# Performance work log

Measured on AMD Instinct MI355X. Metric: run time of the kernel, lower is better.

## Reference

```python
import jax, jax.numpy as jnp
import numpy as np

B, C, H, W = 8, 256, 64, 64
HEADS, R, TOPK_FRAC = 8, 4, 0.25
DIM = C // HEADS
SCALE = DIM ** -0.5


def setup_inputs() -> dict:
    key = jax.random.key(0)
    ks = jax.random.split(key, 8)
    s = 0.05
    return {
        "x": jax.random.normal(ks[0], (B, C, H, W), jnp.float32),
        "w_q": jax.random.normal(ks[1], (C, C), jnp.float32) * s,
        "w_k": jax.random.normal(ks[2], (C, C), jnp.float32) * s,
        "w_v": jax.random.normal(ks[3], (C, C), jnp.float32) * s,
        "w_ck": jax.random.normal(ks[4], (C, R, R), jnp.float32) * s,  # depthwise kxk
        "w_cv": jax.random.normal(ks[5], (C, R, R), jnp.float32) * s,
        "w_out": jax.random.normal(ks[6], (C, C), jnp.float32) * s,
        "b_out": jax.random.normal(ks[7], (C,), jnp.float32) * s,
    }


def _conv1x1(x, w):
    # x: [B,C,H,W], w: [O,C]
    return jnp.einsum('bchw,oc->bohw', x, w)


def _depthwise_pool(x, w):
    # depthwise conv, kernel=stride=R -> non-overlapping blocks
    b, c, h, wd = x.shape
    blocks = x.reshape(b, c, h // R, R, wd // R, R)
    return jnp.einsum('bcirjs,crs->bcij', blocks, w)


def reference(x, w_q, w_k, w_v, w_ck, w_cv, w_out, b_out):
    N = H * W
    q = _conv1x1(x, w_q)
    k = _conv1x1(x, w_k)
    v = _conv1x1(x, w_v)
    k_s = _depthwise_pool(k, w_ck)   # [B,C,H/R,W/R]
    v_s = _depthwise_pool(v, w_cv)
    n = k_s.shape[2] * k_s.shape[3]

    BH = B * HEADS
    q = q.reshape(B, HEADS, DIM, N).reshape(BH, DIM, N)
    k = k_s.reshape(B, HEADS, DIM, n).reshape(BH, DIM, n)
    v = v_s.reshape(B, HEADS, DIM, n).reshape(BH, DIM, n)

    # stage 1: full queries vs compressed keys
    attn = jax.nn.softmax(jnp.einsum('bdi,bdj->bij', q, k) * SCALE, axis=-1)
    token_score = attn.sum(axis=1)                     # [BH, n]
    top_k = max(1, int(n * TOPK_FRAC))
    _, idx = jax.lax.top_k(token_score, top_k)         # [BH, top_k]

    idx_exp = jnp.broadcast_to(idx[:, None, :], (BH, DIM, top_k))
    k_top = jnp.take_along_axis(k, idx_exp, axis=2)    # [BH, DIM, top_k]
    v_top = jnp.take_along_axis(v, idx_exp, axis=2)

    # stage 2: attend only to selected compressed tokens
    attn_full = jax.nn.softmax(jnp.einsum('bdi,bdj->bij', q, k_top) * SCALE, axis=-1)
    out = jnp.einsum('bij,bdj->bdi', attn_full, v_top)  # [BH, DIM, N]
    out = out.reshape(B, HEADS, DIM, N).reshape(B, C, H, W)
    return _conv1x1(out, w_out) + b_out[None, :, None, None]
```

## Files before the change

kernel.cpp:

```cpp
#include <hip/hip_runtime.h>

#define Bq 8
#define Cq 256
#define Hq 64
#define Wq 64
#define Nq 4096
#define HEADSq 8
#define DIMq 32
#define NCq 256
#define TOPKq 64
#define BHq 64
#define SCALEq 0.17677669529663687f

typedef short bf16x8 __attribute__((ext_vector_type(8)));
typedef float f32x4  __attribute__((ext_vector_type(4)));
typedef float f32x16 __attribute__((ext_vector_type(16)));

__device__ __forceinline__ uint32_t f2bf_hi(float f) {
  uint32_t u = __float_as_uint(f);
  return (u + 0x7FFFu + ((u >> 16) & 1u)) >> 16;
}

__device__ __forceinline__ void split8(const float* v, uint4& hv, uint4& lv) {
  uint32_t h[8], l[8];
#pragma unroll
  for (int j = 0; j < 8; ++j) {
    uint32_t hb = f2bf_hi(v[j]);
    float rest = v[j] - __uint_as_float(hb << 16);
    h[j] = hb;
    l[j] = __float_as_uint(rest) >> 16;
  }
  hv = make_uint4(h[0] | (h[1] << 16), h[2] | (h[3] << 16),
                  h[4] | (h[5] << 16), h[6] | (h[7] << 16));
  lv = make_uint4(l[0] | (l[1] << 16), l[2] | (l[3] << 16),
                  l[4] | (l[5] << 16), l[6] | (l[7] << 16));
}


__global__ __launch_bounds__(256) void prep_w(
    const float* __restrict__ wq, const float* __restrict__ wk,
    const float* __restrict__ wv, const float* __restrict__ wo,
    char* __restrict__ wt) {
  const int oblk = blockIdx.x, s = blockIdx.y, mat = blockIdx.z;
  const float* w = mat == 0 ? wq : mat == 1 ? wk : mat == 2 ? wv : wo;
  const int t = threadIdx.x;
  const int o = t & 63, g = t >> 6;
  float v[8];
  const float* src = w + (size_t)(oblk * 64 + o) * Cq + s * 32 + g * 8;
#pragma unroll
  for (int j = 0; j < 8; ++j) v[j] = src[j];
  uint4 hv, lv;
  split8(v, hv, lv);
  size_t base = ((size_t)((mat * 4 + oblk) * 8 + s)) * 8192;
  int off = ((o >> 5) * 2 + (g >> 1)) * 1024 + ((o & 31) + 32 * (g & 1)) * 16;
  *(uint4*)(wt + base + off) = hv;
  *(uint4*)(wt + base + 4096 + off) = lv;
}

__global__ __launch_bounds__(128) void prep_w32(
    const float* __restrict__ wq, const float* __restrict__ wk,
    const float* __restrict__ wv, char* __restrict__ wt32) {
  const int oblk = blockIdx.x, s = blockIdx.y, mat = blockIdx.z;
  const float* w = mat == 0 ? wq : mat == 1 ? wk : wv;
  const int t = threadIdx.x;
  const int o = t & 31, g = t >> 5;
  float v[8];
  const float* src = w + (size_t)(oblk * 32 + o) * Cq + s * 32 + g * 8;
#pragma unroll
  for (int j = 0; j < 8; ++j) v[j] = src[j];
  uint4 hv, lv;
  split8(v, hv, lv);
  size_t base = ((size_t)((mat * 8 + oblk) * 8 + s)) * 4096;
  int off = (g >> 1) * 1024 + (o + 32 * (g & 1)) * 16;
  *(uint4*)(wt32 + base + off) = hv;
  *(uint4*)(wt32 + base + 2048 + off) = lv;
}

__global__ __launch_bounds__(256) void prep_x(
    const float* __restrict__ x, char* __restrict__ xt) {
  const int n64 = blockIdx.x, s = blockIdx.y, b = blockIdx.z;
  const int t = threadIdx.x;
  __shared__ float xf[32][64];
  const float* xb = x + ((size_t)(b * Cq + s * 32)) * Nq + n64 * 64;
#pragma unroll
  for (int ii = 0; ii < 2; ++ii) {
    int e = t + ii * 256;
    int cl = e >> 4, n4 = (e & 15) * 4;
    *(float4*)&xf[cl][n4] = *(const float4*)&xb[(size_t)cl * Nq + n4];
  }
  __syncthreads();
  int n = t & 63, g = t >> 6;
  float v[8];
#pragma unroll
  for (int j = 0; j < 8; ++j) v[j] = xf[g * 8 + j][n];
  uint4 hv, lv;
  split8(v, hv, lv);
  char* dst = xt + ((size_t)((b * 8 + s) * 128 + n64 * 2 + (n >> 5))) * 4096;
  int off = (g >> 1) * 1024 + ((n & 31) + 32 * (g & 1)) * 16;
  *(uint4*)(dst + off) = hv;
  *(uint4*)(dst + 2048 + off) = lv;
}

__global__ __launch_bounds__(256) void qkv_fused(
    const char* __restrict__ wt32, const char* __restrict__ xt,
    const float* __restrict__ wck, const float* __restrict__ wcv,
    char* __restrict__ qimg, float* __restrict__ ksc, float* __restrict__ vsc,
    char* __restrict__ kim) {
  const int i = blockIdx.x, oblk = blockIdx.y, b = blockIdx.z;
  const int t = threadIdx.x, l = t & 63, wid = t >> 6;
  __shared__ __align__(16) short wimg[3][2][1024];
  __shared__ float pp[4][2][32][16];
  __shared__ float wpool[2][32][16];

  for (int u = t; u < 1024; u += 256) {
    int m = u >> 9, c = (u >> 4) & 31, e = u & 15;
    wpool[m][c][e] = (m ? wcv : wck)[(oblk * 32 + c) * 16 + e];
  }

  f32x16 acc[3][2];
#pragma unroll
  for (int m = 0; m < 3; ++m)
#pragma unroll
    for (int nt = 0; nt < 2; ++nt)
#pragma unroll
      for (int r = 0; r < 16; ++r) acc[m][nt][r] = 0.f;

  for (int s = 0; s < 8; ++s) {
    __syncthreads();
#pragma unroll
    for (int u = 0; u < 3; ++u) {
      int e = t + u * 256;
      int m = e >> 8, r = e & 255;
      ((uint4*)&wimg[m][0][0])[r] =
          ((const uint4*)(wt32 + ((size_t)((m * 8 + oblk) * 8 + s)) * 4096))[r];
    }
    __syncthreads();
    bf16x8 xh[2][2], xl[2][2];
#pragma unroll
    for (int nt = 0; nt < 2; ++nt) {
      const char* xb = xt + ((size_t)((b * 8 + s) * 128 + i * 8 + wid * 2 + nt)) * 4096;
#pragma unroll
      for (int kh = 0; kh < 2; ++kh) {
        int off = kh * 1024 + l * 16;
        xh[nt][kh] = *(const bf16x8*)(xb + off);
        xl[nt][kh] = *(const bf16x8*)(xb + 2048 + off);
      }
    }
#pragma unroll
    for (int m = 0; m < 3; ++m)
#pragma unroll
      for (int kh = 0; kh < 2; ++kh) {
        int off = kh * 1024 + l * 16;
        bf16x8 ah = *(const bf16x8*)((const char*)&wimg[m][0][0] + off);
        bf16x8 al = *(const bf16x8*)((const char*)&wimg[m][1][0] + off);
#pragma unroll
        for (int nt = 0; nt < 2; ++nt) {
          acc[m][nt] = __builtin_amdgcn_mfma_f32_32x32x16_bf16(ah, xh[nt][kh], acc[m][nt], 0, 0, 0);
          acc[m][nt] = __builtin_amdgcn_mfma_f32_32x32x16_bf16(ah, xl[nt][kh], acc[m][nt], 0, 0, 0);
          acc[m][nt] = __builtin_amdgcn_mfma_f32_32x32x16_bf16(al, xh[nt][kh], acc[m][nt], 0, 0, 0);
        }
      }
  }

#pragma unroll
  for (int m = 1; m <= 2; ++m)
#pragma unroll
    for (int nt = 0; nt < 2; ++nt)
#pragma unroll
      for (int r = 0; r < 16; ++r) {
        int c_l = (r & 3) + 8 * (r >> 2) + 4 * (l >> 5);
        float sv = acc[m][nt][r] * wpool[m - 1][c_l][wid * 4 + (l & 3)];
        float t0 = sv + __shfl_xor(sv, 1);
        float s4 = t0 + __shfl_xor(t0, 2);
        if ((l & 3) == 0)
          pp[wid][m - 1][c_l][nt * 8 + ((l & 31) >> 2)] = s4;
      }

  const int bh = b * 8 + oblk;
  {
    char* qb = qimg + ((size_t)(bh * 64 + i * 4 + wid)) * 8192;
    const int hi = l >> 5;
#pragma unroll
    for (int nt = 0; nt < 2; ++nt) {
      float sw[16];
#pragma unroll
      for (int r = 0; r < 16; ++r) sw[r] = __shfl_xor(acc[0][nt][r], 32);
      float e0[8], e1[8];
#pragma unroll
      for (int j = 0; j < 4; ++j) {
        e0[j]     = hi ? sw[4 + j]          : acc[0][nt][j];
        e0[4 + j] = hi ? acc[0][nt][4 + j]  : sw[j];
        e1[j]     = hi ? sw[12 + j]         : acc[0][nt][8 + j];
        e1[4 + j] = hi ? acc[0][nt][12 + j] : sw[8 + j];
      }
      uint4 h0, l0v, h1, l1v;
      split8(e0, h0, l0v);
      split8(e1, h1, l1v);
      *(uint4*)(qb + (nt * 2) * 1024 + l * 16) = h0;
      *(uint4*)(qb + 4096 + (nt * 2) * 1024 + l * 16) = l0v;
      *(uint4*)(qb + (nt * 2 + 1) * 1024 + l * 16) = h1;
      *(uint4*)(qb + 4096 + (nt * 2 + 1) * 1024 + l * 16) = l1v;
    }
  }
  __syncthreads();
  float* kpool = &wpool[0][0][0];
  float* vpool = &wpool[1][0][0];
  {
    int c = t >> 3, jj = t & 7;
#pragma unroll
    for (int m = 0; m < 2; ++m)
#pragma unroll
      for (int rep = 0; rep < 2; ++rep) {
        int j = jj + rep * 8;
        float v = pp[0][m][c][j] + pp[1][m][c][j] + pp[2][m][c][j] + pp[3][m][c][j];
        (m ? vpool : kpool)[c * 16 + j] = v;
        float* dst = m ? vsc : ksc;
        dst[((size_t)b * Cq + oblk * 32 + c) * NCq + i * 16 + j] = v;
      }
  }
  __syncthreads();
  if (t < 64) {
    int j = l & 15, g = l >> 4;
    float v[8];
#pragma unroll
    for (int jj = 0; jj < 8; ++jj) v[jj] = kpool[(g * 8 + jj) * 16 + j];
    uint4 hv, lv;
    split8(v, hv, lv);
    char* kb = kim + (size_t)bh * 32768 + i * 1024 + l * 16;
    *(uint4*)kb = hv;
    *(uint4*)(kb + 16384) = lv;
  }
}

__global__ __launch_bounds__(256) void stage1_mfma(
    const char* __restrict__ qim, const char* __restrict__ kim,
    float* __restrict__ part) {
  const int bh = blockIdx.y, chunk = blockIdx.x;
  const int t = threadIdx.x, l = t & 63, wid = t >> 6;
  __shared__ __align__(16) char kimgL[32768];
  __shared__ float sc[4][256];

  {
    const uint4* src = (const uint4*)(kim + (size_t)bh * 32768);
#pragma unroll
    for (int ii = 0; ii < 8; ++ii)
      ((uint4*)kimgL)[t + ii * 256] = src[t + ii * 256];
  }
  float scoreacc[16];
#pragma unroll
  for (int tt = 0; tt < 16; ++tt) scoreacc[tt] = 0.f;
  const int aoff = ((wid >> 1) * 2 + (l >> 5)) * 1024 +
                   ((wid & 1) * 16 + (l & 15) + 32 * ((l >> 4) & 1)) * 16;
  __syncthreads();

#pragma unroll 1
  for (int step = 0; step < 4; ++step) {
    const char* qb = qim + ((size_t)(bh * 64 + chunk * 4 + step)) * 8192;
    bf16x8 ah = *(const bf16x8*)(qb + aoff);
    bf16x8 al = *(const bf16x8*)(qb + 4096 + aoff);
    f32x4 acc[16];
#pragma unroll
    for (int tt = 0; tt < 16; ++tt)
#pragma unroll
      for (int r = 0; r < 4; ++r) acc[tt][r] = 0.f;
#pragma unroll
    for (int tt = 0; tt < 16; ++tt) {
      bf16x8 bhf = *(const bf16x8*)(kimgL + tt * 1024 + l * 16);
      bf16x8 blf = *(const bf16x8*)(kimgL + 16384 + tt * 1024 + l * 16);
      acc[tt] = __builtin_amdgcn_mfma_f32_16x16x32_bf16(ah, bhf, acc[tt], 0, 0, 0);
      acc[tt] = __builtin_amdgcn_mfma_f32_16x16x32_bf16(ah, blf, acc[tt], 0, 0, 0);
      acc[tt] = __builtin_amdgcn_mfma_f32_16x16x32_bf16(al, bhf, acc[tt], 0, 0, 0);
    }
    float mx[4], sm[4];
#pragma unroll
    for (int r = 0; r < 4; ++r) {
      float m = acc[0][r];
#pragma unroll
      for (int tt = 1; tt < 16; ++tt) m = fmaxf(m, acc[tt][r]);
      mx[r] = m;
    }
#pragma unroll
    for (int off = 1; off < 16; off <<= 1)
#pragma unroll
      for (int r = 0; r < 4; ++r) mx[r] = fmaxf(mx[r], __shfl_xor(mx[r], off));
#pragma unroll
    for (int r = 0; r < 4; ++r) sm[r] = 0.f;
#pragma unroll
    for (int tt = 0; tt < 16; ++tt)
#pragma unroll
      for (int r = 0; r < 4; ++r) {
        float e = __expf((acc[tt][r] - mx[r]) * SCALEq);
        acc[tt][r] = e;
        sm[r] += e;
      }
#pragma unroll
    for (int off = 1; off < 16; off <<= 1)
#pragma unroll
      for (int r = 0; r < 4; ++r) sm[r] += __shfl_xor(sm[r], off);
#pragma unroll
    for (int r = 0; r < 4; ++r) sm[r] = 1.0f / sm[r];
#pragma unroll
    for (int tt = 0; tt < 16; ++tt) {
      float tp = acc[tt][0] * sm[0] + acc[tt][1] * sm[1] +
                 acc[tt][2] * sm[2] + acc[tt][3] * sm[3];
      tp += __shfl_xor(tp, 16);
      tp += __shfl_xor(tp, 32);
      scoreacc[tt] += tp;
    }
  }
  if (l < 16) {
#pragma unroll
    for (int tt = 0; tt < 16; ++tt) sc[wid][tt * 16 + l] = scoreacc[tt];
  }
  __syncthreads();
  {
    float v = sc[0][t] + sc[1][t] + sc[2][t] + sc[3][t];
    part[((size_t)bh * 16 + chunk) * NCq + t] = v;
  }
}

__global__ __launch_bounds__(256) void reduce_scores(
    const float* __restrict__ part, float* __restrict__ score) {
  int bh = blockIdx.x, t = threadIdx.x;
  float s = 0.f;
#pragma unroll
  for (int c = 0; c < 16; ++c) s += part[((size_t)bh * 16 + c) * NCq + t];
  score[bh * NCq + t] = s;
}

__global__ __launch_bounds__(256) void topk_sel(
    const float* __restrict__ score, int* __restrict__ idx) {
  int bh = blockIdx.x, t = threadIdx.x;
  __shared__ float s[NCq];
  s[t] = score[bh * NCq + t];
  __syncthreads();
  float st = s[t];
  int rank = 0;
  for (int j = 0; j < NCq; ++j) {
    float sj = s[j];
    rank += (sj > st) || (sj == st && j < t);
  }
  if (rank < TOPKq) idx[bh * TOPKq + rank] = t;
}

__global__ __launch_bounds__(256, 2) void stage2_mfma(
    const char* __restrict__ qim, const float* __restrict__ ks,
    const float* __restrict__ vs, const int* __restrict__ idx,
    char* __restrict__ at) {
  const int bh = blockIdx.y, b = bh >> 3, h = bh & 7;
  const int t = threadIdx.x, l = t & 63, wid = t >> 6;
  __shared__ __align__(16) short kimg[2][2048];
  __shared__ __align__(16) short vimg[2][2][1024];
  __shared__ float pbuf[128][66];
  __shared__ int ibs[64];

  bf16x8 ah[2], al[2];
  {
    const char* qb = qim + ((size_t)(bh * 64 + blockIdx.x * 2 + (wid >> 1))) * 8192;
#pragma unroll
    for (int kd = 0; kd < 2; ++kd) {
      int off = ((wid & 1) * 2 + kd) * 1024 + l * 16;
      ah[kd] = *(const bf16x8*)(qb + off);
      al[kd] = *(const bf16x8*)(qb + 4096 + off);
    }
  }
  const float* ksb = ks + ((size_t)b * Cq + h * DIMq) * NCq;
  const float* vsb = vs + ((size_t)b * Cq + h * DIMq) * NCq;
  if (t < 64) ibs[t] = idx[bh * TOPKq + t];
  __syncthreads();

  {
    int tok = t & 63, dg = t >> 6;
    int ti = ibs[tok];
    float v[8];
#pragma unroll
    for (int j = 0; j < 8; ++j) v[j] = ksb[(size_t)(dg * 8 + j) * NCq + ti];
    uint4 hv, lv;
    split8(v, hv, lv);
    int off = ((tok >> 5) * 2 + (dg >> 1)) * 1024 + ((tok & 31) + 32 * (dg & 1)) * 16;
    *(uint4*)((char*)&kimg[0][0] + off) = hv;
    *(uint4*)((char*)&kimg[1][0] + off) = lv;
  }
  {
    int d = l & 31, tko = l >> 5, img = (t >> 6) >> 1, kreg = (t >> 6) & 1;
    float v[8];
#pragma unroll
    for (int j = 0; j < 8; ++j) {
      int tok = img * 32 + kreg * 16 + tko * 8 + j;
      v[j] = vsb[(size_t)d * NCq + ibs[tok]];
    }
    uint4 hv, lv;
    split8(v, hv, lv);
    int off = kreg * 1024 + (d + 32 * tko) * 16;
    *(uint4*)((char*)&vimg[0][img][0] + off) = hv;
    *(uint4*)((char*)&vimg[1][img][0] + off) = lv;
  }
  __syncthreads();

  f32x16 pacc[2];
#pragma unroll
  for (int g = 0; g < 2; ++g)
#pragma unroll
    for (int r = 0; r < 16; ++r) pacc[g][r] = 0.f;
#pragma unroll
  for (int g = 0; g < 2; ++g)
#pragma unroll
    for (int kd = 0; kd < 2; ++kd) {
      int off = (g * 2 + kd) * 1024 + l * 16;
      bf16x8 bhf = *(const bf16x8*)((const char*)&kimg[0][0] + off);
      bf16x8 blf = *(const bf16x8*)((const char*)&kimg[1][0] + off);
      pacc[g] = __builtin_amdgcn_mfma_f32_32x32x16_bf16(ah[kd], bhf, pacc[g], 0, 0, 0);
      pacc[g] = __builtin_amdgcn_mfma_f32_32x32x16_bf16(ah[kd], blf, pacc[g], 0, 0, 0);
      pacc[g] = __builtin_amdgcn_mfma_f32_32x32x16_bf16(al[kd], bhf, pacc[g], 0, 0, 0);
    }
  {
    float mx[16], sm[16];
#pragma unroll
    for (int r = 0; r < 16; ++r) mx[r] = fmaxf(pacc[0][r], pacc[1][r]);
#pragma unroll
    for (int off = 1; off < 32; off <<= 1)
#pragma unroll
      for (int r = 0; r < 16; ++r) mx[r] = fmaxf(mx[r], __shfl_xor(mx[r], off));
#pragma unroll
    for (int r = 0; r < 16; ++r) {
      float e0 = __expf((pacc[0][r] - mx[r]) * SCALEq);
      float e1 = __expf((pacc[1][r] - mx[r]) * SCALEq);
      pacc[0][r] = e0; pacc[1][r] = e1;
      sm[r] = e0 + e1;
    }
#pragma unroll
    for (int off = 1; off < 32; off <<= 1)
#pragma unroll
      for (int r = 0; r < 16; ++r) sm[r] += __shfl_xor(sm[r], off);
#pragma unroll
    for (int r = 0; r < 16; ++r) sm[r] = 1.0f / sm[r];
#pragma unroll
    for (int g = 0; g < 2; ++g)
#pragma unroll
      for (int r = 0; r < 16; ++r) {
        int qrow = wid * 32 + (r & 3) + 8 * (r >> 2) + 4 * (l >> 5);
        pbuf[qrow][g * 32 + (l & 31)] = pacc[g][r] * sm[r];
      }
  }
  __syncthreads();
  f32x16 oacc;
#pragma unroll
  for (int r = 0; r < 16; ++r) oacc[r] = 0.f;
#pragma unroll
  for (int ks4 = 0; ks4 < 4; ++ks4) {
    const float* pa = &pbuf[wid * 32 + (l & 31)][ks4 * 16 + (l >> 5) * 8];
    float v[8];
#pragma unroll
    for (int j = 0; j < 8; ++j) v[j] = pa[j];
    uint4 hv, lv;
    split8(v, hv, lv);
    bf16x8 pah = *(const bf16x8*)&hv, pal = *(const bf16x8*)&lv;
    int off = (ks4 & 1) * 1024 + l * 16;
    bf16x8 bhf = *(const bf16x8*)((const char*)&vimg[0][ks4 >> 1][0] + off);
    bf16x8 blf = *(const bf16x8*)((const char*)&vimg[1][ks4 >> 1][0] + off);
    oacc = __builtin_amdgcn_mfma_f32_32x32x16_bf16(pah, bhf, oacc, 0, 0, 0);
    oacc = __builtin_amdgcn_mfma_f32_32x32x16_bf16(pah, blf, oacc, 0, 0, 0);
    oacc = __builtin_amdgcn_mfma_f32_32x32x16_bf16(pal, bhf, oacc, 0, 0, 0);
  }
#pragma unroll
  for (int r = 0; r < 16; ++r) {
    int qrow = wid * 32 + (r & 3) + 8 * (r >> 2) + 4 * (l >> 5);
    pbuf[qrow][l & 31] = oacc[r];
  }
  __syncthreads();
#pragma unroll
  for (int ii = 0; ii < 2; ++ii) {
    int slot = t + ii * 256;
    int row = slot >> 2, dg = slot & 3;
    float v[8];
#pragma unroll
    for (int j = 0; j < 8; ++j) v[j] = pbuf[row][dg * 8 + j];
    uint4 hv, lv;
    split8(v, hv, lv);
    int nb = blockIdx.x * 2 + (row >> 6), nloc = row & 63;
    size_t base = ((size_t)((b * 64 + nb) * 8 + h)) * 8192;
    int off = ((nloc >> 5) * 2 + (dg >> 1)) * 1024 +
              ((nloc & 31) + 32 * (dg & 1)) * 16;
    *(uint4*)(at + base + off) = hv;
    *(uint4*)(at + base + 4096 + off) = lv;
  }
}

__global__ __launch_bounds__(256) void out_mfma(
    const char* __restrict__ at, const char* __restrict__ wt,
    const float* __restrict__ bo, float* __restrict__ y) {
  const int b = blockIdx.z, oblk = blockIdx.y, nblk = blockIdx.x;
  const int o0 = oblk * 64, n0 = nblk * 64;
  const int t = threadIdx.x, l = t & 63, wid = t >> 6;
  const int ob = wid >> 1, nbw = wid & 1;
  __shared__ __align__(16) short wimg[2][2048];
  __shared__ __align__(16) short ximg[2][2048];
  __shared__ float bs[64];
  if (t < 64) bs[t] = bo[o0 + t];
  f32x16 acc;
#pragma unroll
  for (int i = 0; i < 16; ++i) acc[i] = 0.f;

  for (int s = 0; s < 8; ++s) {
    __syncthreads();
    {
      const uint4* srcw = (const uint4*)(wt + ((size_t)((12 + oblk) * 8 + s)) * 8192);
      const uint4* srcx = (const uint4*)(at + ((size_t)((b * 64 + nblk) * 8 + s)) * 8192);
#pragma unroll
      for (int i = 0; i < 2; ++i) {
        ((uint4*)&wimg[0][0])[t + i * 256] = srcw[t + i * 256];
        ((uint4*)&ximg[0][0])[t + i * 256] = srcx[t + i * 256];
      }
    }
    __syncthreads();
#pragma unroll
    for (int kh = 0; kh < 2; ++kh) {
      int offa = (ob * 2 + kh) * 1024 + l * 16;
      int offb = (nbw * 2 + kh) * 1024 + l * 16;
      bf16x8 ah = *(const bf16x8*)((const char*)&wimg[0][0] + offa);
      bf16x8 al = *(const bf16x8*)((const char*)&wimg[1][0] + offa);
      bf16x8 bhf = *(const bf16x8*)((const char*)&ximg[0][0] + offb);
      bf16x8 blf = *(const bf16x8*)((const char*)&ximg[1][0] + offb);
      acc = __builtin_amdgcn_mfma_f32_32x32x16_bf16(ah, bhf, acc, 0, 0, 0);
      acc = __builtin_amdgcn_mfma_f32_32x32x16_bf16(ah, blf, acc, 0, 0, 0);
      acc = __builtin_amdgcn_mfma_f32_32x32x16_bf16(al, bhf, acc, 0, 0, 0);
    }
  }
#pragma unroll
  for (int r = 0; r < 16; ++r) {
    int ol = ob * 32 + (r & 3) + 8 * (r >> 2) + 4 * (l >> 5);
    y[((size_t)(b * Cq + o0 + ol)) * Nq + n0 + nbw * 32 + (l & 31)] = acc[r] + bs[ol];
  }
}

extern "C" void kernel_launch(void* const* d_in, const int* in_sizes, int n_in,
                              void* d_out, int out_size, void* d_ws, size_t ws_size,
                              hipStream_t stream) {
  const float* x   = (const float*)d_in[0];
  const float* wq  = (const float*)d_in[1];
  const float* wk  = (const float*)d_in[2];
  const float* wv  = (const float*)d_in[3];
  const float* wck = (const float*)d_in[4];
  const float* wcv = (const float*)d_in[5];
  const float* wo  = (const float*)d_in[6];
  const float* bo  = (const float*)d_in[7];
  float* out = (float*)d_out;

  char* wsb = (char*)d_ws;
  char*  qimg = wsb;
  char*  xt   = wsb + ((size_t)32 << 20);
  char*  at   = xt;
  char*  wt   = wsb + ((size_t)64 << 20);
  char*  wt32 = wsb + ((size_t)65 << 20);
  char*  kim  = wsb + ((size_t)66 << 20);
  float* ksc  = (float*)(wsb + ((size_t)68 << 20));
  float* vsc  = (float*)(wsb + ((size_t)70 << 20));
  float* part = (float*)(wsb + ((size_t)72 << 20));
  float* score= (float*)(wsb + ((size_t)73 << 20));
  int*   idx  = (int*)(wsb + ((size_t)73 << 20) + 65536);

  prep_w<<<dim3(4, 8, 4), 256, 0, stream>>>(wq, wk, wv, wo, wt);
  prep_w32<<<dim3(8, 8, 3), 128, 0, stream>>>(wq, wk, wv, wt32);
  prep_x<<<dim3(64, 8, 8), 256, 0, stream>>>(x, xt);
  qkv_fused<<<dim3(16, 8, 8), 256, 0, stream>>>(wt32, xt, wck, wcv, qimg, ksc, vsc, kim);
  stage1_mfma<<<dim3(16, BHq), 256, 0, stream>>>(qimg, kim, part);
  reduce_scores<<<dim3(BHq), 256, 0, stream>>>(part, score);
  topk_sel<<<dim3(BHq), 256, 0, stream>>>(score, idx);
  stage2_mfma<<<dim3(32, BHq), 256, 0, stream>>>(qimg, ksc, vsc, idx, at);
  out_mfma<<<dim3(64, 4, 8), 256, 0, stream>>>(at, wt, bo, out);
}
```

Measured before the change: 178.5 us.

## Double-buffer weight and activation tiles in QKV and output GEMM kernels

Turns the shared-memory weight tiles in qkv_fused and out_mfma into two-slot ping-pong buffers, and prefetches the next K-slice of weights and activations (into registers for qkv) while MFMAs run on the current slice. Each iteration now needs one barrier instead of two, and global load latency can overlap with matrix math. The cost is doubled LDS for those tiles and extra registers for the prefetched x fragments, which may reduce occupancy. The hi/lo split precision scheme is unchanged.

```diff
diff --git a/kernel.cpp b/kernel.cpp
--- a/kernel.cpp
+++ b/kernel.cpp
@@ -108,7 +108,7 @@
     char* __restrict__ kim) {
   const int i = blockIdx.x, oblk = blockIdx.y, b = blockIdx.z;
   const int t = threadIdx.x, l = t & 63, wid = t >> 6;
-  __shared__ __align__(16) short wimg[3][2][1024];
+  __shared__ __align__(16) short wimg[2][3][2][1024];
   __shared__ float pp[4][2][32][16];
   __shared__ float wpool[2][32][16];
 
@@ -125,40 +125,69 @@
 #pragma unroll
       for (int r = 0; r < 16; ++r) acc[m][nt][r] = 0.f;
 
+  bf16x8 xh[2][2], xl[2][2], nxh[2][2], nxl[2][2];
+#pragma unroll
+  for (int u = 0; u < 3; ++u) {
+    int e = t + u * 256;
+    int m = e >> 8, r = e & 255;
+    ((uint4*)&wimg[0][m][0][0])[r] =
+        ((const uint4*)(wt32 + ((size_t)((m * 8 + oblk) * 8 + 0)) * 4096))[r];
+  }
+#pragma unroll
+  for (int nt = 0; nt < 2; ++nt) {
+    const char* xb = xt + ((size_t)((b * 8 + 0) * 128 + i * 8 + wid * 2 + nt)) * 4096;
+#pragma unroll
+    for (int kh = 0; kh < 2; ++kh) {
+      int off = kh * 1024 + l * 16;
+      xh[nt][kh] = *(const bf16x8*)(xb + off);
+      xl[nt][kh] = *(const bf16x8*)(xb + 2048 + off);
+    }
+  }
+  __syncthreads();
+
+#pragma unroll 1
   for (int s = 0; s < 8; ++s) {
-    __syncthreads();
-#pragma unroll
-    for (int u = 0; u < 3; ++u) {
-      int e = t + u * 256;
-      int m = e >> 8, r = e & 255;
-      ((uint4*)&wimg[m][0][0])[r] =
-          ((const uint4*)(wt32 + ((size_t)((m * 8 + oblk) * 8 + s)) * 4096))[r];
-    }
-    __syncthreads();
-    bf16x8 xh[2][2], xl[2][2];
-#pragma unroll
-    for (int nt = 0; nt < 2; ++nt) {
-      const char* xb = xt + ((size_t)((b * 8 + s) * 128 + i * 8 + wid * 2 + nt)) * 4096;
+    const int cur = s & 1;
+    if (s < 7) {
+#pragma unroll
+      for (int u = 0; u < 3; ++u) {
+        int e = t + u * 256;
+        int m = e >> 8, r = e & 255;
+        ((uint4*)&wimg[cur ^ 1][m][0][0])[r] =
+            ((const uint4*)(wt32 + ((size_t)((m * 8 + oblk) * 8 + s + 1)) * 4096))[r];
+      }
+#pragma unroll
+      for (int nt = 0; nt < 2; ++nt) {
+        const char* xb = xt + ((size_t)((b * 8 + s + 1) * 128 + i * 8 + wid * 2 + nt)) * 4096;
+#pragma unroll
+        for (int kh = 0; kh < 2; ++kh) {
+          int off = kh * 1024 + l * 16;
+          nxh[nt][kh] = *(const bf16x8*)(xb + off);
+          nxl[nt][kh] = *(const bf16x8*)(xb + 2048 + off);
+        }
+      }
+    }
+#pragma unroll
+    for (int m = 0; m < 3; ++m)
 #pragma unroll
       for (int kh = 0; kh < 2; ++kh) {
         int off = kh * 1024 + l * 16;
-        xh[nt][kh] = *(const bf16x8*)(xb + off);
-        xl[nt][kh] = *(const bf16x8*)(xb + 2048 + off);
-      }
-    }
-#pragma unroll
-    for (int m = 0; m < 3; ++m)
-#pragma unroll
-      for (int kh = 0; kh < 2; ++kh) {
-        int off = kh * 1024 + l * 16;
-        bf16x8 ah = *(const bf16x8*)((const char*)&wimg[m][0][0] + off);
-        bf16x8 al = *(const bf16x8*)((const char*)&wimg[m][1][0] + off);
+        bf16x8 ah = *(const bf16x8*)((const char*)&wimg[cur][m][0][0] + off);
+        bf16x8 al = *(const bf16x8*)((const char*)&wimg[cur][m][1][0] + off);
 #pragma unroll
         for (int nt = 0; nt < 2; ++nt) {
           acc[m][nt] = __builtin_amdgcn_mfma_f32_32x32x16_bf16(ah, xh[nt][kh], acc[m][nt], 0, 0, 0);
           acc[m][nt] = __builtin_amdgcn_mfma_f32_32x32x16_bf16(ah, xl[nt][kh], acc[m][nt], 0, 0, 0);
           acc[m][nt] = __builtin_amdgcn_mfma_f32_32x32x16_bf16(al, xh[nt][kh], acc[m][nt], 0, 0, 0);
         }
+      }
+    __syncthreads();
+#pragma unroll
+    for (int nt = 0; nt < 2; ++nt)
+#pragma unroll
+      for (int kh = 0; kh < 2; ++kh) {
+        xh[nt][kh] = nxh[nt][kh];
+        xl[nt][kh] = nxl[nt][kh];
       }
   }
 
@@ -493,38 +522,50 @@
   const int o0 = oblk * 64, n0 = nblk * 64;
   const int t = threadIdx.x, l = t & 63, wid = t >> 6;
   const int ob = wid >> 1, nbw = wid & 1;
-  __shared__ __align__(16) short wimg[2][2048];
-  __shared__ __align__(16) short ximg[2][2048];
+  __shared__ __align__(16) short wimg[2][2][2048];
+  __shared__ __align__(16) short ximg[2][2][2048];
   __shared__ float bs[64];
   if (t < 64) bs[t] = bo[o0 + t];
   f32x16 acc;
 #pragma unroll
   for (int i = 0; i < 16; ++i) acc[i] = 0.f;
 
+  {
+    const uint4* srcw = (const uint4*)(wt + ((size_t)((12 + oblk) * 8 + 0)) * 8192);
+    const uint4* srcx = (const uint4*)(at + ((size_t)((b * 64 + nblk) * 8 + 0)) * 8192);
+#pragma unroll
+    for (int i = 0; i < 2; ++i) {
+      ((uint4*)&wimg[0][0][0])[t + i * 256] = srcw[t + i * 256];
+      ((uint4*)&ximg[0][0][0])[t + i * 256] = srcx[t + i * 256];
+    }
+  }
+  __syncthreads();
+
+#pragma unroll 1
   for (int s = 0; s < 8; ++s) {
-    __syncthreads();
-    {
-      const uint4* srcw = (const uint4*)(wt + ((size_t)((12 + oblk) * 8 + s)) * 8192);
-      const uint4* srcx = (const uint4*)(at + ((size_t)((b * 64 + nblk) * 8 + s)) * 8192);
+    const int cur = s & 1;
+    if (s < 7) {
+      const uint4* srcw = (const uint4*)(wt + ((size_t)((12 + oblk) * 8 + s + 1)) * 8192);
+      const uint4* srcx = (const uint4*)(at + ((size_t)((b * 64 + nblk) * 8 + s + 1)) * 8192);
 #pragma unroll
       for (int i = 0; i < 2; ++i) {
-        ((uint4*)&wimg[0][0])[t + i * 256] = srcw[t + i * 256];
-        ((uint4*)&ximg[0][0])[t + i * 256] = srcx[t + i * 256];
-      }
-    }
-    __syncthreads();
+        ((uint4*)&wimg[cur ^ 1][0][0])[t + i * 256] = srcw[t + i * 256];
+        ((uint4*)&ximg[cur ^ 1][0][0])[t + i * 256] = srcx[t + i * 256];
+      }
+    }
 #pragma unroll
     for (int kh = 0; kh < 2; ++kh) {
       int offa = (ob * 2 + kh) * 1024 + l * 16;
       int offb = (nbw * 2 + kh) * 1024 + l * 16;
-      bf16x8 ah = *(const bf16x8*)((const char*)&wimg[0][0] + offa);
-      bf16x8 al = *(const bf16x8*)((const char*)&wimg[1][0] + offa);
-      bf16x8 bhf = *(const bf16x8*)((const char*)&ximg[0][0] + offb);
-      bf16x8 blf = *(const bf16x8*)((const char*)&ximg[1][0] + offb);
+      bf16x8 ah = *(const bf16x8*)((const char*)&wimg[cur][0][0] + offa);
+      bf16x8 al = *(const bf16x8*)((const char*)&wimg[cur][1][0] + offa);
+      bf16x8 bhf = *(const bf16x8*)((const char*)&ximg[cur][0][0] + offb);
+      bf16x8 blf = *(const bf16x8*)((const char*)&ximg[cur][1][0] + offb);
       acc = __builtin_amdgcn_mfma_f32_32x32x16_bf16(ah, bhf, acc, 0, 0, 0);
       acc = __builtin_amdgcn_mfma_f32_32x32x16_bf16(ah, blf, acc, 0, 0, 0);
       acc = __builtin_amdgcn_mfma_f32_32x32x16_bf16(al, bhf, acc, 0, 0, 0);
     }
+    __syncthreads();
   }
 #pragma unroll
   for (int r = 0; r < 16; ++r) {
```

After: 182.1 us. +2.0%, slower.

## Fuse score reduction into top-k and restructure out projection loads

Applied to the files above, without the earlier changes.

Merges the reduce_scores and topk_sel kernels into a single reduce_topk kernel, which removes one launch and the global round trip of the score buffer. The out_mfma kernel now loads all activation fragments straight from global memory into registers up front. It stages the weight tile through shared memory in two halves instead of syncing twice on every k-step. This cuts synchronisation and LDS traffic but raises register pressure (128 bf16x8 values per thread), which may reduce occupancy.

```diff
diff --git a/kernel.cpp b/kernel.cpp
--- a/kernel.cpp
+++ b/kernel.cpp
@@ -319,20 +319,14 @@
   }
 }
 
-__global__ __launch_bounds__(256) void reduce_scores(
-    const float* __restrict__ part, float* __restrict__ score) {
-  int bh = blockIdx.x, t = threadIdx.x;
-  float s = 0.f;
-#pragma unroll
-  for (int c = 0; c < 16; ++c) s += part[((size_t)bh * 16 + c) * NCq + t];
-  score[bh * NCq + t] = s;
-}
-
-__global__ __launch_bounds__(256) void topk_sel(
-    const float* __restrict__ score, int* __restrict__ idx) {
+__global__ __launch_bounds__(256) void reduce_topk(
+    const float* __restrict__ part, int* __restrict__ idx) {
   int bh = blockIdx.x, t = threadIdx.x;
   __shared__ float s[NCq];
-  s[t] = score[bh * NCq + t];
+  float v = 0.f;
+#pragma unroll
+  for (int c = 0; c < 16; ++c) v += part[((size_t)bh * 16 + c) * NCq + t];
+  s[t] = v;
   __syncthreads();
   float st = s[t];
   int rank = 0;
@@ -493,38 +487,66 @@
   const int o0 = oblk * 64, n0 = nblk * 64;
   const int t = threadIdx.x, l = t & 63, wid = t >> 6;
   const int ob = wid >> 1, nbw = wid & 1;
-  __shared__ __align__(16) short wimg[2][2048];
-  __shared__ __align__(16) short ximg[2][2048];
+  __shared__ __align__(16) char wimg[4][8192];
   __shared__ float bs[64];
   if (t < 64) bs[t] = bo[o0 + t];
+
   f32x16 acc;
 #pragma unroll
   for (int i = 0; i < 16; ++i) acc[i] = 0.f;
 
+  bf16x8 xh[8][2], xl[8][2];
+  const size_t atbase = ((size_t)((b * 64 + nblk) * 8)) * 8192;
+  const int offb0 = (nbw * 2 + 0) * 1024 + l * 16;
+  const int offb1 = (nbw * 2 + 1) * 1024 + l * 16;
+#pragma unroll
   for (int s = 0; s < 8; ++s) {
-    __syncthreads();
-    {
-      const uint4* srcw = (const uint4*)(wt + ((size_t)((12 + oblk) * 8 + s)) * 8192);
-      const uint4* srcx = (const uint4*)(at + ((size_t)((b * 64 + nblk) * 8 + s)) * 8192);
-#pragma unroll
-      for (int i = 0; i < 2; ++i) {
-        ((uint4*)&wimg[0][0])[t + i * 256] = srcw[t + i * 256];
-        ((uint4*)&ximg[0][0])[t + i * 256] = srcx[t + i * 256];
-      }
-    }
-    __syncthreads();
-#pragma unroll
-    for (int kh = 0; kh < 2; ++kh) {
-      int offa = (ob * 2 + kh) * 1024 + l * 16;
-      int offb = (nbw * 2 + kh) * 1024 + l * 16;
-      bf16x8 ah = *(const bf16x8*)((const char*)&wimg[0][0] + offa);
-      bf16x8 al = *(const bf16x8*)((const char*)&wimg[1][0] + offa);
-      bf16x8 bhf = *(const bf16x8*)((const char*)&ximg[0][0] + offb);
-      bf16x8 blf = *(const bf16x8*)((const char*)&ximg[1][0] + offb);
-      acc = __builtin_amdgcn_mfma_f32_32x32x16_bf16(ah, bhf, acc, 0, 0, 0);
-      acc = __builtin_amdgcn_mfma_f32_32x32x16_bf16(ah, blf, acc, 0, 0, 0);
-      acc = __builtin_amdgcn_mfma_f32_32x32x16_bf16(al, bhf, acc, 0, 0, 0);
-    }
+    const char* xb = at + atbase + (size_t)s * 8192;
+    xh[s][0] = *(const bf16x8*)(xb + offb0);
+    xh[s][1] = *(const bf16x8*)(xb + offb1);
+    xl[s][0] = *(const bf16x8*)(xb + 4096 + offb0);
+    xl[s][1] = *(const bf16x8*)(xb + 4096 + offb1);
+  }
+  const uint4* wsrc = (const uint4*)(wt + ((size_t)((12 + oblk) * 8)) * 8192);
+#pragma unroll
+  for (int u = 0; u < 8; ++u)
+    ((uint4*)&wimg[0][0])[t + u * 256] = wsrc[t + u * 256];
+  __syncthreads();
+
+  const int offa0 = (ob * 2 + 0) * 1024 + l * 16;
+  const int offa1 = (ob * 2 + 1) * 1024 + l * 16;
+#pragma unroll
+  for (int s = 0; s < 4; ++s) {
+    const char* wb = wimg[s];
+    bf16x8 ah0 = *(const bf16x8*)(wb + offa0);
+    bf16x8 al0 = *(const bf16x8*)(wb + 4096 + offa0);
+    bf16x8 ah1 = *(const bf16x8*)(wb + offa1);
+    bf16x8 al1 = *(const bf16x8*)(wb + 4096 + offa1);
+    acc = __builtin_amdgcn_mfma_f32_32x32x16_bf16(ah0, xh[s][0], acc, 0, 0, 0);
+    acc = __builtin_amdgcn_mfma_f32_32x32x16_bf16(ah0, xl[s][0], acc, 0, 0, 0);
+    acc = __builtin_amdgcn_mfma_f32_32x32x16_bf16(al0, xh[s][0], acc, 0, 0, 0);
+    acc = __builtin_amdgcn_mfma_f32_32x32x16_bf16(ah1, xh[s][1], acc, 0, 0, 0);
+    acc = __builtin_amdgcn_mfma_f32_32x32x16_bf16(ah1, xl[s][1], acc, 0, 0, 0);
+    acc = __builtin_amdgcn_mfma_f32_32x32x16_bf16(al1, xh[s][1], acc, 0, 0, 0);
+  }
+  __syncthreads();
+#pragma unroll
+  for (int u = 0; u < 8; ++u)
+    ((uint4*)&wimg[0][0])[t + u * 256] = wsrc[2048 + t + u * 256];
+  __syncthreads();
+#pragma unroll
+  for (int s = 4; s < 8; ++s) {
+    const char* wb = wimg[s - 4];
+    bf16x8 ah0 = *(const bf16x8*)(wb + offa0);
+    bf16x8 al0 = *(const bf16x8*)(wb + 4096 + offa0);
+    bf16x8 ah1 = *(const bf16x8*)(wb + offa1);
+    bf16x8 al1 = *(const bf16x8*)(wb + 4096 + offa1);
+    acc = __builtin_amdgcn_mfma_f32_32x32x16_bf16(ah0, xh[s][0], acc, 0, 0, 0);
+    acc = __builtin_amdgcn_mfma_f32_32x32x16_bf16(ah0, xl[s][0], acc, 0, 0, 0);
+    acc = __builtin_amdgcn_mfma_f32_32x32x16_bf16(al0, xh[s][0], acc, 0, 0, 0);
+    acc = __builtin_amdgcn_mfma_f32_32x32x16_bf16(ah1, xh[s][1], acc, 0, 0, 0);
+    acc = __builtin_amdgcn_mfma_f32_32x32x16_bf16(ah1, xl[s][1], acc, 0, 0, 0);
+    acc = __builtin_amdgcn_mfma_f32_32x32x16_bf16(al1, xh[s][1], acc, 0, 0, 0);
   }
 #pragma unroll
   for (int r = 0; r < 16; ++r) {
@@ -556,16 +578,14 @@
   float* ksc  = (float*)(wsb + ((size_t)68 << 20));
   float* vsc  = (float*)(wsb + ((size_t)70 << 20));
   float* part = (float*)(wsb + ((size_t)72 << 20));
-  float* score= (float*)(wsb + ((size_t)73 << 20));
-  int*   idx  = (int*)(wsb + ((size_t)73 << 20) + 65536);
+  int*   idx  = (int*)(wsb + ((size_t)73 << 20));
 
   prep_w<<<dim3(4, 8, 4), 256, 0, stream>>>(wq, wk, wv, wo, wt);
   prep_w32<<<dim3(8, 8, 3), 128, 0, stream>>>(wq, wk, wv, wt32);
   prep_x<<<dim3(64, 8, 8), 256, 0, stream>>>(x, xt);
   qkv_fused<<<dim3(16, 8, 8), 256, 0, stream>>>(wt32, xt, wck, wcv, qimg, ksc, vsc, kim);
   stage1_mfma<<<dim3(16, BHq), 256, 0, stream>>>(qimg, kim, part);
-  reduce_scores<<<dim3(BHq), 256, 0, stream>>>(part, score);
-  topk_sel<<<dim3(BHq), 256, 0, stream>>>(score, idx);
+  reduce_topk<<<dim3(BHq), 256, 0, stream>>>(part, idx);
   stage2_mfma<<<dim3(32, BHq), 256, 0, stream>>>(qimg, ksc, vsc, idx, at);
   out_mfma<<<dim3(64, 4, 8), 256, 0, stream>>>(at, wt, bo, out);
 }
```

Result: no change. 176.6 us (-1.1%).
